# Performance work log

Measured on AMD Instinct MI355X. Metric: run time of the kernel, lower is better.

Reference implementation:

```python
import jax, jax.numpy as jnp
import numpy as np

E = 1024  # n_embd
L = 24    # n_layer
F = 4 * E # ffn hidden

def _ln(x, w, b):
    mu = jnp.mean(x)
    xm = x - mu
    var = jnp.mean(xm * xm)
    return xm * jax.lax.rsqrt(var + 1e-5) * w + b

def setup_inputs() -> dict:
    key = jax.random.key(0)
    ks = jax.random.split(key, 24)
    n = lambda k, s, sc=0.02: jax.random.normal(k, s, dtype=jnp.float32) * sc
    u = lambda k, s, lo, hi: jax.random.uniform(k, s, dtype=jnp.float32, minval=lo, maxval=hi)
    x = jax.random.normal(ks[0], (E,), dtype=jnp.float32)
    statea = jax.random.normal(ks[1], (L, E), dtype=jnp.float32)   # prev ln1 output
    stateb = n(ks[2], (L, E), 0.1)                                  # wkv numerator accum
    statec = u(ks[3], (L, E), 0.5, 1.5)                             # wkv denominator accum (>0)
    stated = jax.random.normal(ks[4], (L, E), dtype=jnp.float32)   # prev ln2 output
    state = jnp.stack([statea, stateb, statec, stated])
    return {
        "x": x,
        "state": state,
        "ln1w": 1.0 + n(ks[5], (L, E)),
        "ln1b": n(ks[6], (L, E)),
        "ln2w": 1.0 + n(ks[7], (L, E)),
        "ln2b": n(ks[8], (L, E)),
        "time_decay": u(ks[9], (L, E), 0.5, 0.99),   # module stores exp(raw) -> positive
        "time_first": u(ks[10], (L, E), 0.1, 1.0),   # module stores exp(raw) -> positive
        "key": n(ks[11], (L, 3, E, E)),              # stack([kk, vv, -rr]) per layer
        "outputv": n(ks[12], (L, E, E)),
        "mix_k": u(ks[13], (L, E), 0.0, 1.0),
        "mix_v": u(ks[14], (L, E), 0.0, 1.0),
        "mix_r": u(ks[15], (L, E), 0.0, 1.0),
        "mix_k_ffn": u(ks[16], (L, E), 0.0, 1.0),
        "mix_r_ffn": u(ks[17], (L, E), 0.0, 1.0),
        "key_ffn": n(ks[18], (L, F, E)),
        "receptance_ffn": n(ks[19], (L, E, E)),      # module stores -w; sign absorbed in init
        "value_ffn": n(ks[20], (L, E, F)),
    }

def reference(x, state, ln1w, ln1b, ln2w, ln2b, time_decay, time_first, key,
              outputv, mix_k, mix_v, mix_r, mix_k_ffn, mix_r_ffn,
              key_ffn, receptance_ffn, value_ffn):
    statea, stateb, statec, stated = state  # each [L, E]
    # forward pre-multiplies time-mix params by the per-layer OLD state (before the loop)
    kktk = mix_k * statea
    vvtv = mix_v * statea
    rrtr = mix_r * statea
    tmk = mix_k_ffn * stated
    tmr = mix_r_ffn * stated

    def step(cx, per):
        (l1w, l1b, l2w, l2b, td, tf, kw, ow, kk, vv, rr, tk, tr,
         kfw, rfw, vfw, sb, sc) = per
        # --- SA (time mixing / WKV state update) ---
        xn = _ln(cx, l1w, l1b)
        k = jnp.exp(kw[0] @ (xn + kk))
        v = kw[1] @ (xn + vv)
        r = jnp.exp(kw[2] @ (xn + rr)) + 1.0   # kw[2] = -rr weight
        wn = sb + tf * k * v
        d = sc * r + tf * k * r
        sx = cx + ow @ (wn / d)
        sb2 = sb * td + k * v
        sc2 = sc * td + k
        # --- FF (channel mixing) ---
        x2 = _ln(sx, l2w, l2b)
        kf = jnp.square(jax.nn.relu(kfw @ (x2 + tk)))
        rf = jnp.exp(rfw @ (x2 + tr))
        out = sx + (vfw @ kf) / (1.0 + rf)
        return out, (xn, sb2, sc2, x2)

    xs = (ln1w, ln1b, ln2w, ln2b, time_decay, time_first, key, outputv,
          kktk, vvtv, rrtr, tmk, tmr, key_ffn, receptance_ffn, value_ffn,
          stateb, statec)
    x_out, (sa, sb, sc, sd) = jax.lax.scan(step, x, xs)
    return x_out, jnp.stack([sa, sb, sc, sd])
```

## Files before the change

kernel.cpp:

```cpp
#include <hip/hip_runtime.h>

#define EDIM 1024
#define LNUM 24
#define FDIM 4096
#define NB 256
#define NT 512

__device__ __forceinline__ float wave_sum(float v) {
#pragma unroll
    for (int off = 32; off > 0; off >>= 1) v += __shfl_xor(v, off, 64);
    return v;
}

__device__ __forceinline__ float2 cload2(const float* p) {
    double d = __hip_atomic_load((const double*)p, __ATOMIC_RELAXED,
                                 __HIP_MEMORY_SCOPE_AGENT);
    float2 r;
    __builtin_memcpy(&r, &d, 8);
    return r;
}
__device__ __forceinline__ float cload1(const float* p) {
    return __hip_atomic_load(p, __ATOMIC_RELAXED, __HIP_MEMORY_SCOPE_AGENT);
}
__device__ __forceinline__ void cstore1(float* p, float v) {
    __hip_atomic_store(p, v, __ATOMIC_RELAXED, __HIP_MEMORY_SCOPE_AGENT);
}

__device__ __forceinline__ void gbar_arrive(unsigned* grp, unsigned* gcnt,
                                            unsigned* rel, unsigned bi) {
    __syncthreads();
    if (threadIdx.x == 0) {
        unsigned o = __hip_atomic_fetch_add(&grp[(blockIdx.x & 7) << 4], 1u,
                                            __ATOMIC_RELAXED, __HIP_MEMORY_SCOPE_AGENT);
        if ((o & 31u) == 31u) {
            unsigned go = __hip_atomic_fetch_add(gcnt, 1u, __ATOMIC_RELAXED,
                                                 __HIP_MEMORY_SCOPE_AGENT);
            if ((go & 7u) == 7u)
                __hip_atomic_store(rel, bi + 1u, __ATOMIC_RELAXED,
                                   __HIP_MEMORY_SCOPE_AGENT);
        }
    }
}

__device__ __forceinline__ void gbar_wait(unsigned* rel, unsigned bi) {
    if (threadIdx.x == 0) {
        int guard = 0;
        while (__hip_atomic_load(rel, __ATOMIC_RELAXED, __HIP_MEMORY_SCOPE_AGENT) <
               bi + 1u) {
            __builtin_amdgcn_s_sleep(1);
            if (++guard > (1 << 20)) break;
        }
    }
    __syncthreads();
}

__device__ __forceinline__ float dot16(const float4& p0, const float4& p1,
                                       const float4& p2, const float4& p3,
                                       const float4& a, const float4& b,
                                       const float4& c, const float4& d) {
    return p0.x * a.x + p0.y * a.y + p0.z * a.z + p0.w * a.w +
           p1.x * b.x + p1.y * b.y + p1.z * b.z + p1.w * b.w +
           p2.x * c.x + p2.y * c.y + p2.z * c.z + p2.w * c.w +
           p3.x * d.x + p3.y * d.y + p3.z * d.z + p3.w * d.w;
}

__device__ __forceinline__ float dot1024_pref(const float4& p0, const float4& p1,
                                              const float4& p2, const float4& p3,
                                              const float* op, int lane) {
    const float4* o = (const float4*)op;
    return wave_sum(dot16(p0, p1, p2, p3, o[lane], o[lane + 64], o[lane + 128],
                          o[lane + 192]));
}

__device__ __forceinline__ float dot512_mem(const float* __restrict__ Wrow,
                                            const float* op, int lane) {
    const float4* q = (const float4*)Wrow;
    const float4* o = (const float4*)op;
    const float4 a = q[lane], b = q[lane + 64];
    const float4 oa = o[lane], ob = o[lane + 64];
    return wave_sum(a.x * oa.x + a.y * oa.y + a.z * oa.z + a.w * oa.w +
                    b.x * ob.x + b.y * ob.y + b.z * ob.z + b.w * ob.w);
}

__device__ __forceinline__ float dot512_pref(const float4& p0, const float4& p1,
                                             const float* op, int lane) {
    const float4* o = (const float4*)op;
    const float4 a = o[lane], b4 = o[lane + 64];
    return wave_sum(p0.x * a.x + p0.y * a.y + p0.z * a.z + p0.w * a.w +
                    p1.x * b4.x + p1.y * b4.y + p1.z * b4.z + p1.w * b4.w);
}

__global__ __launch_bounds__(NT, 2) void rwkv_persistent(
    const float* __restrict__ x_in, const float* __restrict__ state,
    const float* __restrict__ ln1w, const float* __restrict__ ln1b,
    const float* __restrict__ ln2w, const float* __restrict__ ln2b,
    const float* __restrict__ td, const float* __restrict__ tf,
    const float* __restrict__ key, const float* __restrict__ ow,
    const float* __restrict__ mixk, const float* __restrict__ mixv,
    const float* __restrict__ mixr, const float* __restrict__ mixkf,
    const float* __restrict__ mixrf, const float* __restrict__ kffn,
    const float* __restrict__ rffn, const float* __restrict__ vffn,
    float* __restrict__ out, float* __restrict__ ws, unsigned* __restrict__ grp,
    unsigned* __restrict__ gcnt, unsigned* __restrict__ rel) {
    __shared__ float smem[FDIM + 32];
    float* red = smem + FDIM;

    float* xbuf = ws;
    float* sxbuf = ws + 1024;
    float* kbuf = ws + 2048;
    float* vbuf = ws + 3072;
    float* rbuf = ws + 4096;
    float* kfbuf = ws + 5120;
    float* rdiv = ws + 9216;

    float* sa_out = out + EDIM;
    float* sb_out = sa_out + LNUM * EDIM;
    float* sc_out = sb_out + LNUM * EDIM;
    float* sd_out = sc_out + LNUM * EDIM;

    const int t = threadIdx.x;
    const int b = blockIdx.x;
    const int w = t >> 6;
    const int lane = t & 63;
    const int gw = (b << 3) + w;
    unsigned bi = 0;

    float4 pA0, pA1, pA2, pA3;
    {
        const float4* q = (const float4*)(key + ((size_t)gw << 10));
        pA0 = q[lane]; pA1 = q[lane + 64]; pA2 = q[lane + 128]; pA3 = q[lane + 192];
    }

    for (int l = 0; l < LNUM; ++l) {
        const float* cx = (l == 0) ? x_in : xbuf;
        const float* keyl = key + (size_t)l * 3 * EDIM * EDIM;
        const float* owl = ow + (size_t)l * EDIM * EDIM;
        const float* kfl = kffn + (size_t)l * FDIM * EDIM;
        const float* rfl = rffn + (size_t)l * EDIM * EDIM;
        const float* vfl = vffn + (size_t)l * EDIM * FDIM;
        const int le = l * EDIM;

        {
            const float2 xv = cload2(cx + 2 * t);
            float s = xv.x + xv.y, s2 = xv.x * xv.x + xv.y * xv.y;
#pragma unroll
            for (int off = 32; off > 0; off >>= 1) {
                s += __shfl_xor(s, off, 64);
                s2 += __shfl_xor(s2, off, 64);
            }
            if (lane == 0) { red[w] = s; red[8 + w] = s2; }
            __syncthreads();
            float ts = 0.0f, ts2 = 0.0f;
#pragma unroll
            for (int i = 0; i < 8; ++i) { ts += red[i]; ts2 += red[8 + i]; }
            const float mu = ts * (1.0f / 1024.0f);
            const float inv = rsqrtf(ts2 * (1.0f / 1024.0f) - mu * mu + 1e-5f);
            const float2 wv = ((const float2*)(ln1w + le))[t];
            const float2 bv = ((const float2*)(ln1b + le))[t];
            const float2 xn = make_float2((xv.x - mu) * inv * wv.x + bv.x,
                                          (xv.y - mu) * inv * wv.y + bv.y);
            if (b == 0) ((float2*)(sa_out + le))[t] = xn;
            const float2 sav = ((const float2*)(state + le))[t];
            const float2 mk = ((const float2*)(mixk + le))[t];
            const float2 mv = ((const float2*)(mixv + le))[t];
            const float2 mr = ((const float2*)(mixr + le))[t];
            ((float2*)smem)[t] = make_float2(xn.x + mk.x * sav.x, xn.y + mk.y * sav.y);
            ((float2*)(smem + 1024))[t] = make_float2(xn.x + mv.x * sav.x, xn.y + mv.y * sav.y);
            ((float2*)(smem + 2048))[t] = make_float2(xn.x + mr.x * sav.x, xn.y + mr.y * sav.y);
            __syncthreads();
            const int mat = gw >> 10;
            const float d1 = dot1024_pref(pA0, pA1, pA2, pA3, smem + (mat << 10), lane);
            if (lane == 0) {
                if (mat == 0) cstore1(kbuf + gw, expf(d1));
                else          cstore1(vbuf + gw - 1024, d1);
            }
            const int rrow = (b << 2) + (w >> 1);
            const int rh = w & 1;
            const float d2 = dot512_mem(keyl + ((size_t)(2048 + rrow) << 10) + (rh << 9),
                                        smem + 2048 + (rh << 9), lane);
            if (lane == 0) red[16 + w] = d2;
            __syncthreads();
            if (t < 4)
                cstore1(rbuf + (b << 2) + t, expf(red[16 + 2 * t] + red[17 + 2 * t]) + 1.0f);
        }
        gbar_arrive(grp, gcnt, rel, bi);
        float4 pB0, pB1, pC10, pC11, pC12, pC13;
        {
            const float4* qB = (const float4*)(owl + (((b << 2) + (w >> 1)) << 10) +
                                               ((w & 1) << 9));
            pB0 = qB[lane]; pB1 = qB[lane + 64];
            const float4* q1 = (const float4*)(kfl + ((size_t)gw << 10));
            pC10 = q1[lane]; pC11 = q1[lane + 64]; pC12 = q1[lane + 128]; pC13 = q1[lane + 192];
        }
        gbar_wait(rel, bi); ++bi;

        {
            const float2 k2 = cload2(kbuf + 2 * t);
            const float2 v2 = cload2(vbuf + 2 * t);
            const float2 r2 = cload2(rbuf + 2 * t);
            const float2 tf2 = ((const float2*)(tf + le))[t];
            const float2 sb2 = ((const float2*)(state + 1 * LNUM * EDIM + le))[t];
            const float2 sc2 = ((const float2*)(state + 2 * LNUM * EDIM + le))[t];
            const float g0 = (sb2.x + tf2.x * k2.x * v2.x) / (sc2.x * r2.x + tf2.x * k2.x * r2.x);
            const float g1 = (sb2.y + tf2.y * k2.y * v2.y) / (sc2.y * r2.y + tf2.y * k2.y * r2.y);
            ((float2*)smem)[t] = make_float2(g0, g1);
            if (b == 0) {
                const float2 td2 = ((const float2*)(td + le))[t];
                ((float2*)(sb_out + le))[t] =
                    make_float2(sb2.x * td2.x + k2.x * v2.x, sb2.y * td2.y + k2.y * v2.y);
                ((float2*)(sc_out + le))[t] =
                    make_float2(sc2.x * td2.x + k2.x, sc2.y * td2.y + k2.y);
            }
            __syncthreads();
            const float pd = dot512_pref(pB0, pB1, smem + ((w & 1) << 9), lane);
            if (lane == 0) red[w] = pd;
            __syncthreads();
            if (t < 4) {
                const int r = (b << 2) + t;
                cstore1(sxbuf + r, cload1(cx + r) + red[2 * t] + red[2 * t + 1]);
            }
        }
        gbar_arrive(grp, gcnt, rel, bi);
        float4 pC20, pC21, pC22, pC23;
        {
            const float4* q2 = (const float4*)(kfl + ((size_t)(gw + 2048) << 10));
            pC20 = q2[lane]; pC21 = q2[lane + 64]; pC22 = q2[lane + 128]; pC23 = q2[lane + 192];
        }
        gbar_wait(rel, bi); ++bi;

        {
            const float2 sxv = cload2(sxbuf + 2 * t);
            float s = sxv.x + sxv.y, s2 = sxv.x * sxv.x + sxv.y * sxv.y;
#pragma unroll
            for (int off = 32; off > 0; off >>= 1) {
                s += __shfl_xor(s, off, 64);
                s2 += __shfl_xor(s2, off, 64);
            }
            if (lane == 0) { red[w] = s; red[8 + w] = s2; }
            __syncthreads();
            float ts = 0.0f, ts2 = 0.0f;
#pragma unroll
            for (int i = 0; i < 8; ++i) { ts += red[i]; ts2 += red[8 + i]; }
            const float mu = ts * (1.0f / 1024.0f);
            const float inv = rsqrtf(ts2 * (1.0f / 1024.0f) - mu * mu + 1e-5f);
            const float2 wv = ((const float2*)(ln2w + le))[t];
            const float2 bv = ((const float2*)(ln2b + le))[t];
            const float2 x2 = make_float2((sxv.x - mu) * inv * wv.x + bv.x,
                                          (sxv.y - mu) * inv * wv.y + bv.y);
            if (b == 0) ((float2*)(sd_out + le))[t] = x2;
            const float2 sdv = ((const float2*)(state + 3 * LNUM * EDIM + le))[t];
            const float2 mkf = ((const float2*)(mixkf + le))[t];
            const float2 mrf = ((const float2*)(mixrf + le))[t];
            ((float2*)smem)[t] = make_float2(x2.x + mkf.x * sdv.x, x2.y + mkf.y * sdv.y);
            ((float2*)(smem + 1024))[t] = make_float2(x2.x + mrf.x * sdv.x, x2.y + mrf.y * sdv.y);
            __syncthreads();
            const float d1 = dot1024_pref(pC10, pC11, pC12, pC13, smem, lane);
            if (lane == 0) { const float rl = fmaxf(d1, 0.0f); cstore1(kfbuf + gw, rl * rl); }
            const float d2 = dot1024_pref(pC20, pC21, pC22, pC23, smem, lane);
            if (lane == 0) { const float rl = fmaxf(d2, 0.0f); cstore1(kfbuf + gw + 2048, rl * rl); }
            const int rrow = (b << 2) + (w >> 1);
            const int rh = w & 1;
            const float d3 = dot512_mem(rfl + ((size_t)rrow << 10) + (rh << 9),
                                        smem + 1024 + (rh << 9), lane);
            if (lane == 0) red[16 + w] = d3;
            __syncthreads();
            if (t < 4)
                cstore1(rdiv + (b << 2) + t,
                        1.0f / (1.0f + expf(red[16 + 2 * t] + red[17 + 2 * t])));
        }
        gbar_arrive(grp, gcnt, rel, bi);
        const int drow = (b << 2) + (w >> 2);
        const int dch = w & 3;
        float4 pD0, pD1, pD2, pD3, pD4, pD5, pD6, pD7;
        {
            const float4* q1 = (const float4*)(vfl + ((size_t)drow << 12) + (dch << 10));
            pD0 = q1[lane]; pD1 = q1[lane + 64]; pD2 = q1[lane + 128]; pD3 = q1[lane + 192];
            const float4* q2 = (const float4*)(vfl + ((size_t)(drow + 2) << 12) + (dch << 10));
            pD4 = q2[lane]; pD5 = q2[lane + 64]; pD6 = q2[lane + 128]; pD7 = q2[lane + 192];
        }
        gbar_wait(rel, bi); ++bi;

        {
            const double* kfd = (const double*)kfbuf;
#pragma unroll
            for (int j = 0; j < 4; ++j)
                ((double*)smem)[t + j * 512] =
                    __hip_atomic_load(kfd + t + j * 512, __ATOMIC_RELAXED,
                                      __HIP_MEMORY_SCOPE_AGENT);
            __syncthreads();
            const float pd0 = dot1024_pref(pD0, pD1, pD2, pD3, smem + (dch << 10), lane);
            const float pd1 = dot1024_pref(pD4, pD5, pD6, pD7, smem + (dch << 10), lane);
            if (lane == 0) { red[w] = pd0; red[8 + w] = pd1; }
            __syncthreads();
            if (t < 4) {
                const int r = (b << 2) + t;
                const float dsum = red[4 * t] + red[4 * t + 1] + red[4 * t + 2] + red[4 * t + 3];
                const float val = cload1(sxbuf + r) + dsum * cload1(rdiv + r);
                if (l == LNUM - 1) out[r] = val;
                else cstore1(xbuf + r, val);
            }
        }
        if (l < LNUM - 1) {
            gbar_arrive(grp, gcnt, rel, bi);
            const float4* qA = (const float4*)(key + (size_t)(l + 1) * 3 * EDIM * EDIM +
                                               ((size_t)gw << 10));
            pA0 = qA[lane]; pA1 = qA[lane + 64]; pA2 = qA[lane + 128]; pA3 = qA[lane + 192];
            gbar_wait(rel, bi); ++bi;
        }
    }
}

extern "C" void kernel_launch(void* const* d_in, const int* in_sizes, int n_in,
                              void* d_out, int out_size, void* d_ws, size_t ws_size,
                              hipStream_t stream) {
    const float* x_in = (const float*)d_in[0];
    const float* state = (const float*)d_in[1];
    const float* ln1w = (const float*)d_in[2];
    const float* ln1b = (const float*)d_in[3];
    const float* ln2w = (const float*)d_in[4];
    const float* ln2b = (const float*)d_in[5];
    const float* td = (const float*)d_in[6];
    const float* tf = (const float*)d_in[7];
    const float* key = (const float*)d_in[8];
    const float* ow = (const float*)d_in[9];
    const float* mixk = (const float*)d_in[10];
    const float* mixv = (const float*)d_in[11];
    const float* mixr = (const float*)d_in[12];
    const float* mixkf = (const float*)d_in[13];
    const float* mixrf = (const float*)d_in[14];
    const float* kffn = (const float*)d_in[15];
    const float* rffn = (const float*)d_in[16];
    const float* vffn = (const float*)d_in[17];

    float* out = (float*)d_out;
    float* ws = (float*)d_ws;

    unsigned* bar = (unsigned*)((char*)d_ws + 48 * 1024);
    unsigned* grp = bar;
    unsigned* gcnt = bar + 256;
    unsigned* rel = bar + 272;

    hipMemsetAsync(bar, 0, 2048, stream);
    rwkv_persistent<<<NB, NT, 0, stream>>>(x_in, state, ln1w, ln1b, ln2w, ln2b, td, tf,
                                           key, ow, mixk, mixv, mixr, mixkf, mixrf,
                                           kffn, rffn, vffn, out, ws, grp, gcnt, rel);
}
```

Before: 605.2 us.

## Prefetch all weight rows into registers across grid barriers with partial vmcnt waits

Reworks the persistent kernel's grid barrier into a single arrive-and-spin on the group counter, removing the separate release flag and one atomic hop. It issues the receptance rows, both FFN key halves, the FFN receptance rows and the value-FFN rows as register prefetches before each barrier. The barrier waits only on the older memory ops (s_waitcnt vmcnt(N)), so those weight loads stay in flight while the block waits for the others. Local __syncthreads are replaced by raw s_barrier with sched_barrier fences to keep load placement fixed. This raises register pressure and relies on hand-counted vmcnt values being correct.

```diff
diff --git a/kernel.cpp b/kernel.cpp
--- a/kernel.cpp
+++ b/kernel.cpp
@@ -26,32 +26,43 @@
     __hip_atomic_store(p, v, __ATOMIC_RELAXED, __HIP_MEMORY_SCOPE_AGENT);
 }
 
-__device__ __forceinline__ void gbar_arrive(unsigned* grp, unsigned* gcnt,
-                                            unsigned* rel, unsigned bi) {
-    __syncthreads();
+#define FENCE()                                  \
+    do {                                         \
+        asm volatile("" ::: "memory");           \
+        __builtin_amdgcn_sched_barrier(0);       \
+    } while (0)
+
+__device__ __forceinline__ void lbar() {
+    asm volatile("s_waitcnt lgkmcnt(0)" ::: "memory");
+    __builtin_amdgcn_sched_barrier(0);
+    __builtin_amdgcn_s_barrier();
+    asm volatile("" ::: "memory");
+    __builtin_amdgcn_sched_barrier(0);
+}
+
+template <int P>
+__device__ __forceinline__ void gbar(unsigned* grp, unsigned* gcnt, unsigned& bi) {
+    asm volatile("s_waitcnt vmcnt(%0) lgkmcnt(0)" ::"i"(P) : "memory");
+    __builtin_amdgcn_sched_barrier(0);
+    __builtin_amdgcn_s_barrier();
     if (threadIdx.x == 0) {
         unsigned o = __hip_atomic_fetch_add(&grp[(blockIdx.x & 7) << 4], 1u,
                                             __ATOMIC_RELAXED, __HIP_MEMORY_SCOPE_AGENT);
-        if ((o & 31u) == 31u) {
-            unsigned go = __hip_atomic_fetch_add(gcnt, 1u, __ATOMIC_RELAXED,
-                                                 __HIP_MEMORY_SCOPE_AGENT);
-            if ((go & 7u) == 7u)
-                __hip_atomic_store(rel, bi + 1u, __ATOMIC_RELAXED,
+        if ((o & 31u) == 31u)
+            __hip_atomic_fetch_add(gcnt, 1u, __ATOMIC_RELAXED,
                                    __HIP_MEMORY_SCOPE_AGENT);
-        }
-    }
-}
-
-__device__ __forceinline__ void gbar_wait(unsigned* rel, unsigned bi) {
-    if (threadIdx.x == 0) {
+        const unsigned tgt = 8u * (bi + 1u);
         int guard = 0;
-        while (__hip_atomic_load(rel, __ATOMIC_RELAXED, __HIP_MEMORY_SCOPE_AGENT) <
-               bi + 1u) {
+        while (__hip_atomic_load(gcnt, __ATOMIC_RELAXED, __HIP_MEMORY_SCOPE_AGENT) <
+               tgt) {
             __builtin_amdgcn_s_sleep(1);
             if (++guard > (1 << 20)) break;
         }
     }
-    __syncthreads();
+    __builtin_amdgcn_s_barrier();
+    asm volatile("" ::: "memory");
+    __builtin_amdgcn_sched_barrier(0);
+    ++bi;
 }
 
 __device__ __forceinline__ float dot16(const float4& p0, const float4& p1,
@@ -70,16 +81,6 @@
     const float4* o = (const float4*)op;
     return wave_sum(dot16(p0, p1, p2, p3, o[lane], o[lane + 64], o[lane + 128],
                           o[lane + 192]));
-}
-
-__device__ __forceinline__ float dot512_mem(const float* __restrict__ Wrow,
-                                            const float* op, int lane) {
-    const float4* q = (const float4*)Wrow;
-    const float4* o = (const float4*)op;
-    const float4 a = q[lane], b = q[lane + 64];
-    const float4 oa = o[lane], ob = o[lane + 64];
-    return wave_sum(a.x * oa.x + a.y * oa.y + a.z * oa.z + a.w * oa.w +
-                    b.x * ob.x + b.y * ob.y + b.z * ob.z + b.w * ob.w);
 }
 
 __device__ __forceinline__ float dot512_pref(const float4& p0, const float4& p1,
@@ -101,7 +102,7 @@
     const float* __restrict__ mixrf, const float* __restrict__ kffn,
     const float* __restrict__ rffn, const float* __restrict__ vffn,
     float* __restrict__ out, float* __restrict__ ws, unsigned* __restrict__ grp,
-    unsigned* __restrict__ gcnt, unsigned* __restrict__ rel) {
+    unsigned* __restrict__ gcnt) {
     __shared__ float smem[FDIM + 32];
     float* red = smem + FDIM;
 
@@ -123,17 +124,27 @@
     const int w = t >> 6;
     const int lane = t & 63;
     const int gw = (b << 3) + w;
+    const int rrow = (b << 2) + (w >> 1);
+    const int rh = w & 1;
+    const int drow = (b << 2) + (w >> 2);
+    const int dch = w & 3;
     unsigned bi = 0;
 
-    float4 pA0, pA1, pA2, pA3;
+    float4 pA0, pA1, pA2, pA3, rA0, rA1;
+    float4 pB0, pB1;
+    float4 pC10, pC11, pC12, pC13, pC20, pC21, pC22, pC23, rC0, rC1;
+    float4 pD0, pD1, pD2, pD3, pD4, pD5, pD6, pD7;
+
     {
-        const float4* q = (const float4*)(key + ((size_t)gw << 10));
-        pA0 = q[lane]; pA1 = q[lane + 64]; pA2 = q[lane + 128]; pA3 = q[lane + 192];
+        const float4* qA = (const float4*)(key + ((size_t)gw << 10));
+        pA0 = qA[lane]; pA1 = qA[lane + 64]; pA2 = qA[lane + 128]; pA3 = qA[lane + 192];
+        const float4* qR =
+            (const float4*)(key + ((size_t)(2048 + rrow) << 10) + (rh << 9));
+        rA0 = qR[lane]; rA1 = qR[lane + 64];
     }
 
     for (int l = 0; l < LNUM; ++l) {
         const float* cx = (l == 0) ? x_in : xbuf;
-        const float* keyl = key + (size_t)l * 3 * EDIM * EDIM;
         const float* owl = ow + (size_t)l * EDIM * EDIM;
         const float* kfl = kffn + (size_t)l * FDIM * EDIM;
         const float* rfl = rffn + (size_t)l * EDIM * EDIM;
@@ -149,7 +160,7 @@
                 s2 += __shfl_xor(s2, off, 64);
             }
             if (lane == 0) { red[w] = s; red[8 + w] = s2; }
-            __syncthreads();
+            lbar();
             float ts = 0.0f, ts2 = 0.0f;
 #pragma unroll
             for (int i = 0; i < 8; ++i) { ts += red[i]; ts2 += red[8 + i]; }
@@ -165,34 +176,36 @@
             const float2 mv = ((const float2*)(mixv + le))[t];
             const float2 mr = ((const float2*)(mixr + le))[t];
             ((float2*)smem)[t] = make_float2(xn.x + mk.x * sav.x, xn.y + mk.y * sav.y);
-            ((float2*)(smem + 1024))[t] = make_float2(xn.x + mv.x * sav.x, xn.y + mv.y * sav.y);
-            ((float2*)(smem + 2048))[t] = make_float2(xn.x + mr.x * sav.x, xn.y + mr.y * sav.y);
-            __syncthreads();
+            ((float2*)(smem + 1024))[t] =
+                make_float2(xn.x + mv.x * sav.x, xn.y + mv.y * sav.y);
+            ((float2*)(smem + 2048))[t] =
+                make_float2(xn.x + mr.x * sav.x, xn.y + mr.y * sav.y);
+            lbar();
             const int mat = gw >> 10;
             const float d1 = dot1024_pref(pA0, pA1, pA2, pA3, smem + (mat << 10), lane);
             if (lane == 0) {
                 if (mat == 0) cstore1(kbuf + gw, expf(d1));
                 else          cstore1(vbuf + gw - 1024, d1);
             }
-            const int rrow = (b << 2) + (w >> 1);
-            const int rh = w & 1;
-            const float d2 = dot512_mem(keyl + ((size_t)(2048 + rrow) << 10) + (rh << 9),
-                                        smem + 2048 + (rh << 9), lane);
+            const float d2 = dot512_pref(rA0, rA1, smem + 2048 + (rh << 9), lane);
             if (lane == 0) red[16 + w] = d2;
-            __syncthreads();
+            lbar();
             if (t < 4)
-                cstore1(rbuf + (b << 2) + t, expf(red[16 + 2 * t] + red[17 + 2 * t]) + 1.0f);
-        }
-        gbar_arrive(grp, gcnt, rel, bi);
-        float4 pB0, pB1, pC10, pC11, pC12, pC13;
-        {
-            const float4* qB = (const float4*)(owl + (((b << 2) + (w >> 1)) << 10) +
-                                               ((w & 1) << 9));
+                cstore1(rbuf + (b << 2) + t,
+                        expf(red[16 + 2 * t] + red[17 + 2 * t]) + 1.0f);
+        }
+        FENCE();
+        {
+            const float4* qB = (const float4*)(owl + ((size_t)rrow << 10) + (rh << 9));
             pB0 = qB[lane]; pB1 = qB[lane + 64];
             const float4* q1 = (const float4*)(kfl + ((size_t)gw << 10));
             pC10 = q1[lane]; pC11 = q1[lane + 64]; pC12 = q1[lane + 128]; pC13 = q1[lane + 192];
-        }
-        gbar_wait(rel, bi); ++bi;
+            const float4* q2 = (const float4*)(kfl + ((size_t)(gw + 2048) << 10));
+            pC20 = q2[lane]; pC21 = q2[lane + 64]; pC22 = q2[lane + 128]; pC23 = q2[lane + 192];
+            const float4* qR = (const float4*)(rfl + ((size_t)rrow << 10) + (rh << 9));
+            rC0 = qR[lane]; rC1 = qR[lane + 64];
+        }
+        gbar<12>(grp, gcnt, bi);
 
         {
             const float2 k2 = cload2(kbuf + 2 * t);
@@ -201,8 +214,10 @@
             const float2 tf2 = ((const float2*)(tf + le))[t];
             const float2 sb2 = ((const float2*)(state + 1 * LNUM * EDIM + le))[t];
             const float2 sc2 = ((const float2*)(state + 2 * LNUM * EDIM + le))[t];
-            const float g0 = (sb2.x + tf2.x * k2.x * v2.x) / (sc2.x * r2.x + tf2.x * k2.x * r2.x);
-            const float g1 = (sb2.y + tf2.y * k2.y * v2.y) / (sc2.y * r2.y + tf2.y * k2.y * r2.y);
+            const float g0 =
+                (sb2.x + tf2.x * k2.x * v2.x) / (sc2.x * r2.x + tf2.x * k2.x * r2.x);
+            const float g1 =
+                (sb2.y + tf2.y * k2.y * v2.y) / (sc2.y * r2.y + tf2.y * k2.y * r2.y);
             ((float2*)smem)[t] = make_float2(g0, g1);
             if (b == 0) {
                 const float2 td2 = ((const float2*)(td + le))[t];
@@ -211,22 +226,24 @@
                 ((float2*)(sc_out + le))[t] =
                     make_float2(sc2.x * td2.x + k2.x, sc2.y * td2.y + k2.y);
             }
-            __syncthreads();
-            const float pd = dot512_pref(pB0, pB1, smem + ((w & 1) << 9), lane);
+            lbar();
+            const float pd = dot512_pref(pB0, pB1, smem + (rh << 9), lane);
             if (lane == 0) red[w] = pd;
-            __syncthreads();
+            lbar();
             if (t < 4) {
                 const int r = (b << 2) + t;
                 cstore1(sxbuf + r, cload1(cx + r) + red[2 * t] + red[2 * t + 1]);
             }
         }
-        gbar_arrive(grp, gcnt, rel, bi);
-        float4 pC20, pC21, pC22, pC23;
-        {
-            const float4* q2 = (const float4*)(kfl + ((size_t)(gw + 2048) << 10));
-            pC20 = q2[lane]; pC21 = q2[lane + 64]; pC22 = q2[lane + 128]; pC23 = q2[lane + 192];
-        }
-        gbar_wait(rel, bi); ++bi;
+        FENCE();
+        {
+            const float4* q1 = (const float4*)(vfl + ((size_t)drow << 12) + (dch << 10));
+            pD0 = q1[lane]; pD1 = q1[lane + 64]; pD2 = q1[lane + 128]; pD3 = q1[lane + 192];
+            const float4* q2 =
+                (const float4*)(vfl + ((size_t)(drow + 2) << 12) + (dch << 10));
+            pD4 = q2[lane]; pD5 = q2[lane + 64]; pD6 = q2[lane + 128]; pD7 = q2[lane + 192];
+        }
+        gbar<8>(grp, gcnt, bi);
 
         {
             const float2 sxv = cload2(sxbuf + 2 * t);
@@ -237,7 +254,7 @@
                 s2 += __shfl_xor(s2, off, 64);
             }
             if (lane == 0) { red[w] = s; red[8 + w] = s2; }
-            __syncthreads();
+            lbar();
             float ts = 0.0f, ts2 = 0.0f;
 #pragma unroll
             for (int i = 0; i < 8; ++i) { ts += red[i]; ts2 += red[8 + i]; }
@@ -252,60 +269,53 @@
             const float2 mkf = ((const float2*)(mixkf + le))[t];
             const float2 mrf = ((const float2*)(mixrf + le))[t];
             ((float2*)smem)[t] = make_float2(x2.x + mkf.x * sdv.x, x2.y + mkf.y * sdv.y);
-            ((float2*)(smem + 1024))[t] = make_float2(x2.x + mrf.x * sdv.x, x2.y + mrf.y * sdv.y);
-            __syncthreads();
+            ((float2*)(smem + 1024))[t] =
+                make_float2(x2.x + mrf.x * sdv.x, x2.y + mrf.y * sdv.y);
+            lbar();
             const float d1 = dot1024_pref(pC10, pC11, pC12, pC13, smem, lane);
             if (lane == 0) { const float rl = fmaxf(d1, 0.0f); cstore1(kfbuf + gw, rl * rl); }
             const float d2 = dot1024_pref(pC20, pC21, pC22, pC23, smem, lane);
             if (lane == 0) { const float rl = fmaxf(d2, 0.0f); cstore1(kfbuf + gw + 2048, rl * rl); }
-            const int rrow = (b << 2) + (w >> 1);
-            const int rh = w & 1;
-            const float d3 = dot512_mem(rfl + ((size_t)rrow << 10) + (rh << 9),
-                                        smem + 1024 + (rh << 9), lane);
+            const float d3 = dot512_pref(rC0, rC1, smem + 1024 + (rh << 9), lane);
             if (lane == 0) red[16 + w] = d3;
-            __syncthreads();
+            lbar();
             if (t < 4)
                 cstore1(rdiv + (b << 2) + t,
                         1.0f / (1.0f + expf(red[16 + 2 * t] + red[17 + 2 * t])));
         }
-        gbar_arrive(grp, gcnt, rel, bi);
-        const int drow = (b << 2) + (w >> 2);
-        const int dch = w & 3;
-        float4 pD0, pD1, pD2, pD3, pD4, pD5, pD6, pD7;
-        {
-            const float4* q1 = (const float4*)(vfl + ((size_t)drow << 12) + (dch << 10));
-            pD0 = q1[lane]; pD1 = q1[lane + 64]; pD2 = q1[lane + 128]; pD3 = q1[lane + 192];
-            const float4* q2 = (const float4*)(vfl + ((size_t)(drow + 2) << 12) + (dch << 10));
-            pD4 = q2[lane]; pD5 = q2[lane + 64]; pD6 = q2[lane + 128]; pD7 = q2[lane + 192];
-        }
-        gbar_wait(rel, bi); ++bi;
+        gbar<0>(grp, gcnt, bi);
 
         {
             const double* kfd = (const double*)kfbuf;
 #pragma unroll
             for (int j = 0; j < 4; ++j)
-                ((double*)smem)[t + j * 512] =
-                    __hip_atomic_load(kfd + t + j * 512, __ATOMIC_RELAXED,
-                                      __HIP_MEMORY_SCOPE_AGENT);
-            __syncthreads();
+                ((double*)smem)[t + j * 512] = __hip_atomic_load(
+                    kfd + t + j * 512, __ATOMIC_RELAXED, __HIP_MEMORY_SCOPE_AGENT);
+            lbar();
             const float pd0 = dot1024_pref(pD0, pD1, pD2, pD3, smem + (dch << 10), lane);
             const float pd1 = dot1024_pref(pD4, pD5, pD6, pD7, smem + (dch << 10), lane);
             if (lane == 0) { red[w] = pd0; red[8 + w] = pd1; }
-            __syncthreads();
+            lbar();
             if (t < 4) {
                 const int r = (b << 2) + t;
-                const float dsum = red[4 * t] + red[4 * t + 1] + red[4 * t + 2] + red[4 * t + 3];
+                const float dsum =
+                    red[4 * t] + red[4 * t + 1] + red[4 * t + 2] + red[4 * t + 3];
                 const float val = cload1(sxbuf + r) + dsum * cload1(rdiv + r);
                 if (l == LNUM - 1) out[r] = val;
                 else cstore1(xbuf + r, val);
             }
         }
         if (l < LNUM - 1) {
-            gbar_arrive(grp, gcnt, rel, bi);
-            const float4* qA = (const float4*)(key + (size_t)(l + 1) * 3 * EDIM * EDIM +
-                                               ((size_t)gw << 10));
-            pA0 = qA[lane]; pA1 = qA[lane + 64]; pA2 = qA[lane + 128]; pA3 = qA[lane + 192];
-            gbar_wait(rel, bi); ++bi;
+            FENCE();
+            {
+                const float* keyn = key + (size_t)(l + 1) * 3 * EDIM * EDIM;
+                const float4* qA = (const float4*)(keyn + ((size_t)gw << 10));
+                pA0 = qA[lane]; pA1 = qA[lane + 64]; pA2 = qA[lane + 128]; pA3 = qA[lane + 192];
+                const float4* qR =
+                    (const float4*)(keyn + ((size_t)(2048 + rrow) << 10) + (rh << 9));
+                rA0 = qR[lane]; rA1 = qR[lane + 64];
+            }
+            gbar<6>(grp, gcnt, bi);
         }
     }
 }
@@ -338,10 +348,9 @@
     unsigned* bar = (unsigned*)((char*)d_ws + 48 * 1024);
     unsigned* grp = bar;
     unsigned* gcnt = bar + 256;
-    unsigned* rel = bar + 272;
 
     hipMemsetAsync(bar, 0, 2048, stream);
     rwkv_persistent<<<NB, NT, 0, stream>>>(x_in, state, ln1w, ln1b, ln2w, ln2b, td, tf,
                                            key, ow, mixk, mixv, mixr, mixkf, mixrf,
-                                           kffn, rffn, vffn, out, ws, grp, gcnt, rel);
-}
+                                           kffn, rffn, vffn, out, ws, grp, gcnt);
+}
```

New measurement: 604.9 us. Within noise of the previous version (-0.1%).
